# Kernel tuning notes

Measured on AMD Instinct MI355X. Metric: run time of the kernel, lower is better.

## Reference

```python
import jax, jax.numpy as jnp
import numpy as np

DEPTH = 8
N_FEATURES = 512
N_CLASSES = 1000
N_LEAVES = 2 ** DEPTH          # 256
N_INTERNAL = N_LEAVES - 1      # 255
BATCH = 16384


def _path_tables():
    """Static routing tables for a complete binary tree (heap indexing).

    nodes[d, l] = internal node index visited at level d on the path to leaf l
    bits[d, l]  = 1 if path goes right at that node, else 0
    """
    leaves = np.arange(N_LEAVES)
    nodes = np.stack([(2 ** d - 1) + (leaves >> (DEPTH - d)) for d in range(DEPTH)])
    bits = np.stack([(leaves >> (DEPTH - 1 - d)) & 1 for d in range(DEPTH)])
    return nodes, bits


_NODES, _BITS = _path_tables()


def setup_inputs() -> dict:
    key = jax.random.key(0)
    k1, k2, k3 = jax.random.split(key, 3)
    x = jax.random.normal(k1, (BATCH, N_FEATURES), dtype=jnp.float32)
    # xavier-uniform-ish scale for the stacked gate weights
    gate_w = jax.random.normal(k2, (N_INTERNAL, N_FEATURES), dtype=jnp.float32) / np.sqrt(N_FEATURES)
    gate_b = jnp.zeros((N_INTERNAL,), dtype=jnp.float32)
    leaf_logits = jax.random.normal(k3, (N_LEAVES, N_CLASSES), dtype=jnp.float32) * 0.1
    return {"x": x, "gate_w": gate_w, "gate_b": gate_b, "leaf_logits": leaf_logits}


def reference(x, gate_w, gate_b, leaf_logits):
    # All internal-node gates as one batched matmul: [B, N_INTERNAL]
    p_right = jax.nn.sigmoid(jnp.einsum("bf,nf->bn", x, gate_w) + gate_b)
    # Arrival probability of each leaf: product of branch probs along its path.
    mu = jnp.ones((x.shape[0], N_LEAVES), dtype=x.dtype)
    for d in range(DEPTH):  # static loop over tree depth (8 iters)
        g = p_right[:, _NODES[d]]                       # [B, N_LEAVES]
        branch = jnp.where(_BITS[d] == 1, g, 1.0 - g)   # right vs left prob
        mu = mu * branch
    # Leaf class distributions: softmax per leaf over classes
    leaf_dists = jax.nn.softmax(leaf_logits, axis=-1)   # [N_LEAVES, N_CLASSES]
    return mu @ leaf_dists                              # [B, N_CLASSES]
```

## Files before the change

kernel.cpp:

```cpp
#include <hip/hip_runtime.h>

typedef __attribute__((ext_vector_type(8))) _Float16 f16x8;
typedef __attribute__((ext_vector_type(4))) _Float16 f16x4;
typedef __attribute__((ext_vector_type(4))) float   f32x4;

#define BATCH 16384
#define NFEAT 512
#define NCLS  1000
#define NLEAF 256
#define NINT  255
#define LDP   72
#define PSTR  257

__global__ __launch_bounds__(64) void cvt_gw(const float* __restrict__ gw,
                                             _Float16* __restrict__ gwF) {
  const int p = blockIdx.x;
  const int lane = threadIdx.x;
  const int c = (p >> 4) * 16 + (lane & 15);
  const int k0 = (p & 15) * 32 + (lane >> 4) * 8;
  f16x8 o = {};
  if (c < NINT) {
    float4 v0 = *(const float4*)&gw[(size_t)c * NFEAT + k0];
    float4 v1 = *(const float4*)&gw[(size_t)c * NFEAT + k0 + 4];
    o[0] = (_Float16)v0.x; o[1] = (_Float16)v0.y;
    o[2] = (_Float16)v0.z; o[3] = (_Float16)v0.w;
    o[4] = (_Float16)v1.x; o[5] = (_Float16)v1.y;
    o[6] = (_Float16)v1.z; o[7] = (_Float16)v1.w;
  }
  *(f16x8*)&gwF[((size_t)p * 64 + lane) * 8] = o;
}

__global__ __launch_bounds__(256) void softmax_t(const float* __restrict__ L,
                                                 _Float16* __restrict__ distF) {
  __shared__ float red[4];
  const int l = blockIdx.x, t = threadIdx.x;
  const int wave = t >> 6, lane = t & 63;
  const int kt = l >> 5, lhi_l = (l >> 3) & 3, jj = l & 7;
  float v[4];
  const bool live = t < 250;
  if (live) {
    float4 f = *(const float4*)&L[(size_t)l * NCLS + t * 4];
    v[0] = f.x; v[1] = f.y; v[2] = f.z; v[3] = f.w;
  } else {
    v[0] = v[1] = v[2] = v[3] = -1e30f;
  }
  float mx = fmaxf(fmaxf(v[0], v[1]), fmaxf(v[2], v[3]));
#pragma unroll
  for (int s = 32; s; s >>= 1) mx = fmaxf(mx, __shfl_xor(mx, s));
  if (lane == 0) red[wave] = mx;
  __syncthreads();
  mx = fmaxf(fmaxf(red[0], red[1]), fmaxf(red[2], red[3]));
  __syncthreads();
  float e[4], sum = 0.f;
#pragma unroll
  for (int i = 0; i < 4; ++i) { e[i] = __expf(v[i] - mx); sum += e[i]; }
  if (!live) { e[0] = e[1] = e[2] = e[3] = 0.f; sum = 0.f; }
#pragma unroll
  for (int s = 32; s; s >>= 1) sum += __shfl_xor(sum, s);
  if (lane == 0) red[wave] = sum;
  __syncthreads();
  sum = red[0] + red[1] + red[2] + red[3];
  float inv = 1.f / sum;
#pragma unroll
  for (int i = 0; i < 4; ++i) {
    int c = t * 4 + i;
    float val = live ? e[i] * inv : 0.f;
    int c16 = c >> 4, ln = c & 15;
    size_t idx = (((size_t)(c16 * 8 + kt)) * 64 + lhi_l * 16 + ln) * 8 + jj;
    distF[idx] = (_Float16)val;
  }
}

__global__ __launch_bounds__(512)
void g1mu(const float* __restrict__ x, const _Float16* __restrict__ gwF,
          const float* __restrict__ gb, _Float16* __restrict__ muFg) {
  __shared__ union {
    _Float16 A[32 * LDP];
    float P[32 * PSTR];
  } sm;

  const int tid  = threadIdx.x;
  const int wave = tid >> 6, lane = tid & 63;
  const int ln15 = lane & 15, lhi = lane >> 4;
  const int wr = wave >> 2, wc = wave & 3;
  const int r0 = blockIdx.x * 32;

  f32x4 acc1[4] = {};
  const int arow = tid >> 4, acol = (tid & 15) * 4;

  float4 pa = *(const float4*)&x[(size_t)(r0 + arow) * NFEAT + acol];
  for (int k = 0; k < NFEAT / 64; ++k) {
    {
      f16x4 h;
      h[0] = (_Float16)pa.x; h[1] = (_Float16)pa.y;
      h[2] = (_Float16)pa.z; h[3] = (_Float16)pa.w;
      *(f16x4*)&sm.A[arow * LDP + acol] = h;
    }
    __syncthreads();
    if (k < NFEAT / 64 - 1)
      pa = *(const float4*)&x[(size_t)(r0 + arow) * NFEAT + (k + 1) * 64 + acol];
#pragma unroll
    for (int kk = 0; kk < 2; ++kk) {
      f16x8 a = *(const f16x8*)&sm.A[(wr * 16 + ln15) * LDP + kk * 32 + lhi * 8];
#pragma unroll
      for (int n = 0; n < 4; ++n) {
        f16x8 b = *(const f16x8*)&gwF[(((size_t)(wc * 4 + n) * 16 + k * 2 + kk) * 64 + lane) * 8];
        acc1[n] = __builtin_amdgcn_mfma_f32_16x16x32_f16(a, b, acc1[n], 0, 0, 0);
      }
    }
    __syncthreads();
  }

#pragma unroll
  for (int n = 0; n < 4; ++n) {
    int col = wc * 64 + n * 16 + ln15;
    float bb = (col < NINT) ? gb[col] : 0.f;
#pragma unroll
    for (int j = 0; j < 4; ++j) {
      int rl = wr * 16 + lhi * 4 + j;
      float v = acc1[n][j] + bb;
      sm.P[rl * PSTR + col] = 1.f / (1.f + __expf(-v));
    }
  }
  __syncthreads();

  const int lf   = lane * 4;
  const int g_hi = lane >> 3;
  const int sub  = ((lane >> 1) & 3) * 16;
  const int j4   = (lane & 1) * 4;
#pragma unroll
  for (int rr = 0; rr < 4; ++rr) {
    int row = wave * 4 + rr;
    const float* p = &sm.P[row * PSTR];
    float pre = 1.f;
#pragma unroll
    for (int d = 0; d < 6; ++d) {
      int node = (1 << d) - 1 + (lf >> (8 - d));
      int bit  = (lf >> (7 - d)) & 1;
      float g = p[node];
      pre *= bit ? g : (1.f - g);
    }
    float g6  = p[63 + lane];
    float g7a = p[127 + 2 * lane];
    float g7b = p[128 + 2 * lane];
    f16x4 o;
    o[0] = (_Float16)(pre * (1.f - g6) * (1.f - g7a));
    o[1] = (_Float16)(pre * (1.f - g6) * g7a);
    o[2] = (_Float16)(pre * g6 * (1.f - g7b));
    o[3] = (_Float16)(pre * g6 * g7b);
    int row_g = r0 + row;
    size_t idx = (((size_t)(row_g >> 4) * 8 + g_hi) * 64 + sub + (row_g & 15)) * 8 + j4;
    *(f16x4*)&muFg[idx] = o;
  }
}

__global__ __launch_bounds__(256)
void g2(const _Float16* __restrict__ muFg, const _Float16* __restrict__ distF,
        float* __restrict__ out) {
  __shared__ _Float16 sMu[4 * 8 * 64 * 8];
  const int tid  = threadIdx.x;
  const int wave = tid >> 6, lane = tid & 63;
  const int ln15 = lane & 15, lhi = lane >> 4;
  const int bx = blockIdx.x;
  const int by = blockIdx.y;

  {
    const f16x8* src = (const f16x8*)(muFg + (size_t)bx * 16384);
    f16x8* dst = (f16x8*)sMu;
#pragma unroll
    for (int i = 0; i < 8; ++i)
      dst[tid + i * 256] = src[tid + i * 256];
  }
  __syncthreads();

  for (int h = 0; h < 4; ++h) {
    const int c16 = by * 16 + wave * 4 + h;
    f16x8 bb[8];
#pragma unroll
    for (int kk = 0; kk < 8; ++kk)
      bb[kk] = *(const f16x8*)&distF[(((size_t)c16 * 8 + kk) * 64 + lane) * 8];
#pragma unroll
    for (int g = 0; g < 4; ++g) {
      f32x4 acc = {};
#pragma unroll
      for (int kk = 0; kk < 8; ++kk) {
        f16x8 aa = *(const f16x8*)&sMu[((g * 8 + kk) * 64 + lane) * 8];
        acc = __builtin_amdgcn_mfma_f32_16x16x32_f16(bb[kk], aa, acc, 0, 0, 0);
      }
      const int brow = (bx * 4 + g) * 16 + ln15;
      const int col4 = c16 * 16 + lhi * 4;
      if (col4 < NCLS)
        *(f32x4*)&out[(size_t)brow * NCLS + col4] = acc;
    }
  }
}

extern "C" void kernel_launch(void* const* d_in, const int* in_sizes, int n_in,
                              void* d_out, int out_size, void* d_ws, size_t ws_size,
                              hipStream_t stream) {
  const float* x  = (const float*)d_in[0];
  const float* gw = (const float*)d_in[1];
  const float* gb = (const float*)d_in[2];
  const float* ll = (const float*)d_in[3];
  float* out = (float*)d_out;
  char* ws = (char*)d_ws;

  _Float16* gwF   = (_Float16*)(ws);
  _Float16* distF = (_Float16*)(ws + 262144);
  _Float16* muFg  = (_Float16*)(ws + 786432);

  cvt_gw   <<<256, 64,  0, stream>>>(gw, gwF);
  softmax_t<<<256, 256, 0, stream>>>(ll, distF);
  g1mu     <<<BATCH / 32, 512, 0, stream>>>(x, gwF, gb, muFg);
  g2       <<<dim3(BATCH / 64, 4), 256, 0, stream>>>(muFg, distF, out);
}
```

Before: 56.28 us.

## Widen gate GEMM tile to 64 rows per block and merge prep kernels

The gate-GEMM kernel now processes 64 batch rows per 1024-thread block. Each of 16 waves owns one 16-column slice of the gate weights and covers all four row tiles, so each weight fragment loaded from global memory is reused across four MFMAs instead of one. The weight fp16 conversion and the leaf softmax are merged into a single launch by splitting on block index, which removes one kernel launch. In exchange the block uses more LDS (about 66 KB) and there are half as many blocks, which may reduce latency hiding and load balance across CUs.

```diff
diff --git a/kernel.cpp b/kernel.cpp
--- a/kernel.cpp
+++ b/kernel.cpp
@@ -12,29 +12,30 @@
 #define LDP   72
 #define PSTR  257
 
-__global__ __launch_bounds__(64) void cvt_gw(const float* __restrict__ gw,
-                                             _Float16* __restrict__ gwF) {
-  const int p = blockIdx.x;
-  const int lane = threadIdx.x;
-  const int c = (p >> 4) * 16 + (lane & 15);
-  const int k0 = (p & 15) * 32 + (lane >> 4) * 8;
-  f16x8 o = {};
-  if (c < NINT) {
-    float4 v0 = *(const float4*)&gw[(size_t)c * NFEAT + k0];
-    float4 v1 = *(const float4*)&gw[(size_t)c * NFEAT + k0 + 4];
-    o[0] = (_Float16)v0.x; o[1] = (_Float16)v0.y;
-    o[2] = (_Float16)v0.z; o[3] = (_Float16)v0.w;
-    o[4] = (_Float16)v1.x; o[5] = (_Float16)v1.y;
-    o[6] = (_Float16)v1.z; o[7] = (_Float16)v1.w;
-  }
-  *(f16x8*)&gwF[((size_t)p * 64 + lane) * 8] = o;
-}
-
-__global__ __launch_bounds__(256) void softmax_t(const float* __restrict__ L,
-                                                 _Float16* __restrict__ distF) {
+__global__ __launch_bounds__(256) void prep(const float* __restrict__ L,
+                                            _Float16* __restrict__ distF,
+                                            const float* __restrict__ gw,
+                                            _Float16* __restrict__ gwF) {
+  const int t = threadIdx.x;
+  const int wave = t >> 6, lane = t & 63;
+  if (blockIdx.x >= 256) {
+    const int p = (blockIdx.x - 256) * 4 + wave;
+    const int c = (p >> 4) * 16 + (lane & 15);
+    const int k0 = (p & 15) * 32 + (lane >> 4) * 8;
+    f16x8 o = {};
+    if (c < NINT) {
+      float4 v0 = *(const float4*)&gw[(size_t)c * NFEAT + k0];
+      float4 v1 = *(const float4*)&gw[(size_t)c * NFEAT + k0 + 4];
+      o[0] = (_Float16)v0.x; o[1] = (_Float16)v0.y;
+      o[2] = (_Float16)v0.z; o[3] = (_Float16)v0.w;
+      o[4] = (_Float16)v1.x; o[5] = (_Float16)v1.y;
+      o[6] = (_Float16)v1.z; o[7] = (_Float16)v1.w;
+    }
+    *(f16x8*)&gwF[((size_t)p * 64 + lane) * 8] = o;
+    return;
+  }
   __shared__ float red[4];
-  const int l = blockIdx.x, t = threadIdx.x;
-  const int wave = t >> 6, lane = t & 63;
+  const int l = blockIdx.x;
   const int kt = l >> 5, lhi_l = (l >> 3) & 3, jj = l & 7;
   float v[4];
   const bool live = t < 250;
@@ -71,19 +72,18 @@
   }
 }
 
-__global__ __launch_bounds__(512)
+__global__ __launch_bounds__(1024)
 void g1mu(const float* __restrict__ x, const _Float16* __restrict__ gwF,
           const float* __restrict__ gb, _Float16* __restrict__ muFg) {
   __shared__ union {
-    _Float16 A[32 * LDP];
-    float P[32 * PSTR];
+    _Float16 A[64 * LDP];
+    float P[64 * PSTR];
   } sm;
 
   const int tid  = threadIdx.x;
   const int wave = tid >> 6, lane = tid & 63;
   const int ln15 = lane & 15, lhi = lane >> 4;
-  const int wr = wave >> 2, wc = wave & 3;
-  const int r0 = blockIdx.x * 32;
+  const int r0 = blockIdx.x * 64;
 
   f32x4 acc1[4] = {};
   const int arow = tid >> 4, acol = (tid & 15) * 4;
@@ -101,26 +101,29 @@
       pa = *(const float4*)&x[(size_t)(r0 + arow) * NFEAT + (k + 1) * 64 + acol];
 #pragma unroll
     for (int kk = 0; kk < 2; ++kk) {
-      f16x8 a = *(const f16x8*)&sm.A[(wr * 16 + ln15) * LDP + kk * 32 + lhi * 8];
-#pragma unroll
-      for (int n = 0; n < 4; ++n) {
-        f16x8 b = *(const f16x8*)&gwF[(((size_t)(wc * 4 + n) * 16 + k * 2 + kk) * 64 + lane) * 8];
-        acc1[n] = __builtin_amdgcn_mfma_f32_16x16x32_f16(a, b, acc1[n], 0, 0, 0);
+      f16x8 a[4];
+#pragma unroll
+      for (int m = 0; m < 4; ++m)
+        a[m] = *(const f16x8*)&sm.A[(m * 16 + ln15) * LDP + kk * 32 + lhi * 8];
+      f16x8 b = *(const f16x8*)&gwF[(((size_t)wave * 16 + k * 2 + kk) * 64 + lane) * 8];
+#pragma unroll
+      for (int m = 0; m < 4; ++m)
+        acc1[m] = __builtin_amdgcn_mfma_f32_16x16x32_f16(a[m], b, acc1[m], 0, 0, 0);
+    }
+    __syncthreads();
+  }
+
+  {
+    int col = wave * 16 + ln15;
+    float bb = (col < NINT) ? gb[col] : 0.f;
+#pragma unroll
+    for (int m = 0; m < 4; ++m)
+#pragma unroll
+      for (int j = 0; j < 4; ++j) {
+        int rl = m * 16 + lhi * 4 + j;
+        float v = acc1[m][j] + bb;
+        sm.P[rl * PSTR + col] = 1.f / (1.f + __expf(-v));
       }
-    }
-    __syncthreads();
-  }
-
-#pragma unroll
-  for (int n = 0; n < 4; ++n) {
-    int col = wc * 64 + n * 16 + ln15;
-    float bb = (col < NINT) ? gb[col] : 0.f;
-#pragma unroll
-    for (int j = 0; j < 4; ++j) {
-      int rl = wr * 16 + lhi * 4 + j;
-      float v = acc1[n][j] + bb;
-      sm.P[rl * PSTR + col] = 1.f / (1.f + __expf(-v));
-    }
   }
   __syncthreads();
 
@@ -209,8 +212,7 @@
   _Float16* distF = (_Float16*)(ws + 262144);
   _Float16* muFg  = (_Float16*)(ws + 786432);
 
-  cvt_gw   <<<256, 64,  0, stream>>>(gw, gwF);
-  softmax_t<<<256, 256, 0, stream>>>(ll, distF);
-  g1mu     <<<BATCH / 32, 512, 0, stream>>>(x, gwF, gb, muFg);
-  g2       <<<dim3(BATCH / 64, 4), 256, 0, stream>>>(muFg, distF, out);
-}
+  prep <<<320, 256, 0, stream>>>(ll, distF, gw, gwF);
+  g1mu <<<BATCH / 64, 1024, 0, stream>>>(x, gwF, gb, muFg);
+  g2   <<<dim3(BATCH / 64, 4), 256, 0, stream>>>(muFg, distF, out);
+}
```

Measured after the change: 53.79 us (median of 2 runs). 1.05x faster.
